# Kernel optimization log

Hardware: AMD Instinct MI355X
Metric: run time of the kernel (lower is better)

The kernel has to match this reference:

```python
import jax, jax.numpy as jnp
import numpy as np

E = 160000
N_NODES = 10000
AVG_NUM_NEIGHBORS = 16.0
INV_SQRT3 = 0.5773502691896258  # CG normalization for 1o x 1o -> 0e


def setup_inputs() -> dict:
    key = jax.random.key(0)
    ks = jax.random.split(key, 12)
    d = {
        "edge_s": jax.random.normal(ks[0], (E, 64), jnp.float32),
        "edge_v": jax.random.normal(ks[1], (E, 64, 3), jnp.float32),
        "attr_s": jax.random.normal(ks[2], (E, 1), jnp.float32),
        "attr_v": jax.random.normal(ks[3], (E, 3), jnp.float32),
        "W1": jax.random.normal(ks[4], (64, 128), jnp.float32) / np.sqrt(64),
        "b1": jnp.zeros((128,), jnp.float32),
        "W2": jax.random.normal(ks[5], (128, 128), jnp.float32) / np.sqrt(128),
        "b2": jnp.zeros((128,), jnp.float32),
        "Wg": jax.random.normal(ks[6], (128, 256), jnp.float32) / np.sqrt(128),
        "bg": jnp.zeros((256,), jnp.float32),
        "receivers": jax.random.randint(ks[7], (E,), 0, N_NODES, jnp.int32),
        "n_nodes": N_NODES,
    }
    return d


def reference(edge_s, edge_v, attr_s, attr_v, W1, b1, W2, b2, Wg, bg, receivers, n_nodes):
    # --- equivariant tensor product (filtered to 0e + 1o) ---
    # 0e outputs: [0e x 0e -> 0e (64)] ++ [1o x 1o -> 0e (64)]
    m0 = jnp.concatenate(
        [edge_s * attr_s,
         jnp.einsum("evc,ec->ev", edge_v, attr_v) * INV_SQRT3],
        axis=-1)                                            # [E, 128]
    # 1o outputs: [0e x 1o -> 1o (64)] ++ [1o x 0e -> 1o (64)]
    m1 = jnp.concatenate(
        [edge_s[:, :, None] * attr_v[:, None, :],
         edge_v * attr_s[:, :, None]],
        axis=1)                                             # [E, 128, 3]

    # --- scalar MLP gate (activate_final=True) + Linear to num_irreps=256 ---
    h = jax.nn.silu(edge_s @ W1 + b1)
    h = jax.nn.silu(h @ W2 + b2)
    gate = h @ Wg + bg                                      # [E, 256]
    g0, g1 = gate[:, :128], gate[:, 128:]

    m0 = m0 * g0
    m1 = m1 * g1[:, :, None]

    # --- scatter-add aggregation over receivers ---
    node0 = jax.ops.segment_sum(m0, receivers, num_segments=n_nodes)   # [N, 128]
    node1 = jax.ops.segment_sum(
        m1.reshape(m1.shape[0], -1), receivers, num_segments=n_nodes)  # [N, 384]

    out = jnp.concatenate([node0, node1], axis=-1)          # [N, 512]
    return out / jnp.sqrt(jnp.float32(AVG_NUM_NEIGHBORS))
```

## Files before the change

### kernel.cpp

```cpp
#include <hip/hip_runtime.h>
#include <math.h>

#define EPB 16
#define MEPB 32
#define NTHREADS 256
#define SCAN_T 1024
#define MAX_NODES_SCAN 10240
#define INV_SQRT3f 0.57735026918962584f
#define WFRAG_BYTES (112 * 1024)

typedef short bf16x8 __attribute__((ext_vector_type(8)));
typedef float f32x4  __attribute__((ext_vector_type(4)));

__device__ __forceinline__ float silu_f(float x) {
    return x * (1.0f / (1.0f + __expf(-x)));
}

__device__ __forceinline__ unsigned short f2bf(float f) {
    union { float f; unsigned u; } c; c.f = f;
    unsigned u = c.u + 0x7FFFu + ((c.u >> 16) & 1u);
    return (unsigned short)(u >> 16);
}

__global__ __launch_bounds__(64)
void wprep(const float* __restrict__ W1, const float* __restrict__ W2,
           const float* __restrict__ Wg, short* __restrict__ wf) {
    const int fid = blockIdx.x;
    const int l = threadIdx.x;
    const float* W; int N, nt, kt;
    if (fid < 16)      { W = W1; N = 128; nt = fid >> 1;        kt = fid & 1; }
    else if (fid < 48) { W = W2; N = 128; nt = (fid - 16) >> 2; kt = (fid - 16) & 3; }
    else               { W = Wg; N = 256; nt = (fid - 48) >> 2; kt = (fid - 48) & 3; }
    const int col = nt * 16 + (l & 15);
    const int k0  = kt * 32 + (l >> 4) * 8;
    short* out = wf + fid * 512 + l * 8;
    #pragma unroll
    for (int j = 0; j < 8; ++j)
        out[j] = (short)f2bf(W[(k0 + j) * N + col]);
}

__global__ __launch_bounds__(NTHREADS)
void mlp_gate_mfma(const float* __restrict__ edge_s,
                   const float* __restrict__ b1,
                   const float* __restrict__ b2,
                   const float* __restrict__ bg,
                   const short* __restrict__ wf,
                   float* __restrict__ gate_out,
                   int E)
{
    __shared__ alignas(16) char h_lds[2][32 * 256];

    const int tid = threadIdx.x;
    const int w  = tid >> 6;
    const int l  = tid & 63;
    const int lg = l >> 4;
    const int lc = l & 15;
    const long e0 = (long)blockIdx.x * MEPB;
    if (e0 + MEPB > E) return;

    bf16x8 a1[2][2];
    #pragma unroll
    for (int mt = 0; mt < 2; ++mt)
        #pragma unroll
        for (int kt = 0; kt < 2; ++kt) {
            const float* p = edge_s + (e0 + mt * 16 + lc) * 64 + kt * 32 + lg * 8;
            float4 x0 = *(const float4*)p;
            float4 x1 = *(const float4*)(p + 4);
            bf16x8 a;
            a[0] = (short)f2bf(x0.x); a[1] = (short)f2bf(x0.y);
            a[2] = (short)f2bf(x0.z); a[3] = (short)f2bf(x0.w);
            a[4] = (short)f2bf(x1.x); a[5] = (short)f2bf(x1.y);
            a[6] = (short)f2bf(x1.z); a[7] = (short)f2bf(x1.w);
            a1[mt][kt] = a;
        }

    {
        bf16x8 bw[2][2];
        #pragma unroll
        for (int nt = 0; nt < 2; ++nt)
            #pragma unroll
            for (int kt = 0; kt < 2; ++kt)
                bw[nt][kt] = *(const bf16x8*)(wf + ((2 * w + nt) * 2 + kt) * 512 + l * 8);

        f32x4 acc[2][2];
        #pragma unroll
        for (int mt = 0; mt < 2; ++mt)
            #pragma unroll
            for (int nt = 0; nt < 2; ++nt) {
                f32x4 c = {0.f, 0.f, 0.f, 0.f};
                #pragma unroll
                for (int kt = 0; kt < 2; ++kt)
                    c = __builtin_amdgcn_mfma_f32_16x16x32_bf16(a1[mt][kt], bw[nt][kt], c, 0, 0, 0);
                acc[mt][nt] = c;
            }

        #pragma unroll
        for (int nt = 0; nt < 2; ++nt) {
            float bb = b1[32 * w + nt * 16 + lc];
            int col2 = (32 * w + nt * 16 + lc) * 2;
            #pragma unroll
            for (int mt = 0; mt < 2; ++mt)
                #pragma unroll
                for (int r = 0; r < 4; ++r) {
                    int row = mt * 16 + lg * 4 + r;
                    int off = (row * 256 + col2) ^ ((row & 7) << 4);
                    *(unsigned short*)&h_lds[0][off] = f2bf(silu_f(acc[mt][nt][r] + bb));
                }
        }
    }
    __syncthreads();

    {
        bf16x8 a2[2][4];
        #pragma unroll
        for (int mt = 0; mt < 2; ++mt)
            #pragma unroll
            for (int kt = 0; kt < 4; ++kt) {
                int row = mt * 16 + lc;
                int off = (row * 256 + (kt * 32 + lg * 8) * 2) ^ ((row & 7) << 4);
                a2[mt][kt] = *(const bf16x8*)&h_lds[0][off];
            }

        f32x4 acc[2][2];
        #pragma unroll
        for (int mt = 0; mt < 2; ++mt)
            #pragma unroll
            for (int nt = 0; nt < 2; ++nt) { f32x4 z = {0.f,0.f,0.f,0.f}; acc[mt][nt] = z; }

        #pragma unroll
        for (int kt = 0; kt < 4; ++kt) {
            bf16x8 bw[2];
            #pragma unroll
            for (int nt = 0; nt < 2; ++nt)
                bw[nt] = *(const bf16x8*)(wf + (16 + (2 * w + nt) * 4 + kt) * 512 + l * 8);
            #pragma unroll
            for (int mt = 0; mt < 2; ++mt)
                #pragma unroll
                for (int nt = 0; nt < 2; ++nt)
                    acc[mt][nt] = __builtin_amdgcn_mfma_f32_16x16x32_bf16(a2[mt][kt], bw[nt], acc[mt][nt], 0, 0, 0);
        }

        #pragma unroll
        for (int nt = 0; nt < 2; ++nt) {
            float bb = b2[32 * w + nt * 16 + lc];
            int col2 = (32 * w + nt * 16 + lc) * 2;
            #pragma unroll
            for (int mt = 0; mt < 2; ++mt)
                #pragma unroll
                for (int r = 0; r < 4; ++r) {
                    int row = mt * 16 + lg * 4 + r;
                    int off = (row * 256 + col2) ^ ((row & 7) << 4);
                    *(unsigned short*)&h_lds[1][off] = f2bf(silu_f(acc[mt][nt][r] + bb));
                }
        }
    }
    __syncthreads();

    {
        bf16x8 a3[2][4];
        #pragma unroll
        for (int mt = 0; mt < 2; ++mt)
            #pragma unroll
            for (int kt = 0; kt < 4; ++kt) {
                int row = mt * 16 + lc;
                int off = (row * 256 + (kt * 32 + lg * 8) * 2) ^ ((row & 7) << 4);
                a3[mt][kt] = *(const bf16x8*)&h_lds[1][off];
            }

        f32x4 acc[2][4];
        #pragma unroll
        for (int mt = 0; mt < 2; ++mt)
            #pragma unroll
            for (int nt = 0; nt < 4; ++nt) { f32x4 z = {0.f,0.f,0.f,0.f}; acc[mt][nt] = z; }

        #pragma unroll
        for (int kt = 0; kt < 4; ++kt) {
            bf16x8 bw[4];
            #pragma unroll
            for (int nt = 0; nt < 4; ++nt)
                bw[nt] = *(const bf16x8*)(wf + (48 + (4 * w + nt) * 4 + kt) * 512 + l * 8);
            #pragma unroll
            for (int mt = 0; mt < 2; ++mt)
                #pragma unroll
                for (int nt = 0; nt < 4; ++nt)
                    acc[mt][nt] = __builtin_amdgcn_mfma_f32_16x16x32_bf16(a3[mt][kt], bw[nt], acc[mt][nt], 0, 0, 0);
        }

        #pragma unroll
        for (int nt = 0; nt < 4; ++nt) {
            int col = 64 * w + nt * 16 + lc;
            float bb = bg[col];
            #pragma unroll
            for (int mt = 0; mt < 2; ++mt)
                #pragma unroll
                for (int r = 0; r < 4; ++r) {
                    long e = e0 + mt * 16 + lg * 4 + r;
                    gate_out[e * 256 + col] = (acc[mt][nt][r] + bb) * 0.25f;
                }
        }
    }
}

__global__ void csr_hist(const int* __restrict__ recv, int* __restrict__ counts, int E) {
    int e = blockIdx.x * 256 + threadIdx.x;
    if (e < E) atomicAdd(&counts[recv[e]], 1);
}

__global__ __launch_bounds__(SCAN_T)
void csr_scan(const int* __restrict__ counts, int* __restrict__ offsets,
              int* __restrict__ cursor, int N) {
    __shared__ int s_cnt[MAX_NODES_SCAN];
    __shared__ int s_ps[SCAN_T];
    const int t = threadIdx.x;
    for (int i = t; i < N; i += SCAN_T) s_cnt[i] = counts[i];
    __syncthreads();
    const int CH = (N + SCAN_T - 1) / SCAN_T;
    const int base = t * CH;
    int tsum = 0;
    for (int k = 0; k < CH; ++k) { int i = base + k; if (i < N) tsum += s_cnt[i]; }
    s_ps[t] = tsum;
    __syncthreads();
    for (int off = 1; off < SCAN_T; off <<= 1) {
        int v = (t >= off) ? s_ps[t - off] : 0;
        __syncthreads();
        s_ps[t] += v;
        __syncthreads();
    }
    int run = (t == 0) ? 0 : s_ps[t - 1];
    for (int k = 0; k < CH; ++k) {
        int i = base + k;
        if (i < N) { int c = s_cnt[i]; offsets[i] = run; cursor[i] = run; run += c; }
    }
    if (t == 0) offsets[N] = s_ps[SCAN_T - 1];
}

__global__ void csr_scatter(const int* __restrict__ recv, int* __restrict__ cursor,
                            int* __restrict__ eids, int E) {
    int e = blockIdx.x * 256 + threadIdx.x;
    if (e < E) {
        int p = atomicAdd(&cursor[recv[e]], 1);
        eids[p] = e;
    }
}

__global__ __launch_bounds__(NTHREADS)
void node_gather(const float* __restrict__ edge_s,
                 const float* __restrict__ edge_v,
                 const float* __restrict__ attr_s,
                 const float* __restrict__ attr_v,
                 const float* __restrict__ gate,
                 const int*   __restrict__ offsets,
                 const int*   __restrict__ eids,
                 float* __restrict__ out)
{
    __shared__ int s_ids[NTHREADS];
    const int n   = blockIdx.x;
    const int tid = threadIdx.x;
    const int start = offsets[n];
    const int end   = offsets[n + 1];
    const int i = tid - 128;

    float  acc0 = 0.0f;
    float3 acc1 = make_float3(0.0f, 0.0f, 0.0f);

    for (int base = start; base < end; base += NTHREADS) {
        const int cnt = min(NTHREADS, end - base);
        __syncthreads();
        if (tid < cnt) s_ids[tid] = eids[base + tid];
        __syncthreads();
        for (int p = 0; p < cnt; ++p) {
            const int e = s_ids[p];
            const float as  = attr_s[e];
            const float av0 = attr_v[e * 3 + 0];
            const float av1 = attr_v[e * 3 + 1];
            const float av2 = attr_v[e * 3 + 2];
            const float g   = gate[(size_t)e * 256 + tid];
            if (tid < 64) {
                acc0 = fmaf(edge_s[(size_t)e * 64 + tid] * as, g, acc0);
            } else if (tid < 128) {
                const float* ev = &edge_v[((size_t)e * 64 + (tid - 64)) * 3];
                float val = (ev[0] * av0 + ev[1] * av1 + ev[2] * av2) * INV_SQRT3f;
                acc0 = fmaf(val, g, acc0);
            } else if (i < 64) {
                float es = edge_s[(size_t)e * 64 + i];
                acc1.x = fmaf(es * av0, g, acc1.x);
                acc1.y = fmaf(es * av1, g, acc1.y);
                acc1.z = fmaf(es * av2, g, acc1.z);
            } else {
                const float* ev = &edge_v[((size_t)e * 64 + (i - 64)) * 3];
                acc1.x = fmaf(ev[0] * as, g, acc1.x);
                acc1.y = fmaf(ev[1] * as, g, acc1.y);
                acc1.z = fmaf(ev[2] * as, g, acc1.z);
            }
        }
    }

    float* orow = out + (size_t)n * 512;
    if (tid < 128) {
        orow[tid] = acc0;
    } else {
        orow[128 + 3 * i + 0] = acc1.x;
        orow[128 + 3 * i + 1] = acc1.y;
        orow[128 + 3 * i + 2] = acc1.z;
    }
}

__global__ __launch_bounds__(NTHREADS)
void mpconv_fused_atomic(const float* __restrict__ edge_s,
                         const float* __restrict__ edge_v,
                         const float* __restrict__ attr_s,
                         const float* __restrict__ attr_v,
                         const float* __restrict__ W1, const float* __restrict__ b1,
                         const float* __restrict__ W2, const float* __restrict__ b2,
                         const float* __restrict__ Wg, const float* __restrict__ bg,
                         const int*   __restrict__ recv,
                         float* __restrict__ out)
{
    __shared__ float s_esT[64][20];
    __shared__ float s_h1T[128][20];
    __shared__ float s_h2T[128][20];
    __shared__ float s_as[EPB];
    __shared__ float s_av[EPB][3];
    __shared__ int   s_r[EPB];

    const int tid = threadIdx.x;
    const long e0 = (long)blockIdx.x * EPB;

    for (int idx = tid; idx < EPB * 64; idx += NTHREADS) {
        int e = idx >> 6, k = idx & 63;
        s_esT[k][e] = edge_s[(e0 + e) * 64 + k];
    }
    if (tid < EPB) { s_as[tid] = attr_s[e0 + tid]; s_r[tid] = recv[e0 + tid]; }
    if (tid >= 64 && tid < 64 + EPB * 3) {
        int q = tid - 64; int e = q / 3, c = q - e * 3;
        s_av[e][c] = attr_v[(e0 + e) * 3 + c];
    }
    __syncthreads();

    const int j  = tid & 127;
    const int eg = (tid >> 7) << 3;
    {
        float acc[8];
        #pragma unroll
        for (int e = 0; e < 8; ++e) acc[e] = 0.0f;
        #pragma unroll 4
        for (int k = 0; k < 64; ++k) {
            float w  = W1[k * 128 + j];
            float4 a = *(const float4*)&s_esT[k][eg];
            float4 b = *(const float4*)&s_esT[k][eg + 4];
            acc[0] = fmaf(a.x, w, acc[0]); acc[1] = fmaf(a.y, w, acc[1]);
            acc[2] = fmaf(a.z, w, acc[2]); acc[3] = fmaf(a.w, w, acc[3]);
            acc[4] = fmaf(b.x, w, acc[4]); acc[5] = fmaf(b.y, w, acc[5]);
            acc[6] = fmaf(b.z, w, acc[6]); acc[7] = fmaf(b.w, w, acc[7]);
        }
        float bb = b1[j];
        float4 r0, r1;
        r0.x = silu_f(acc[0] + bb); r0.y = silu_f(acc[1] + bb);
        r0.z = silu_f(acc[2] + bb); r0.w = silu_f(acc[3] + bb);
        r1.x = silu_f(acc[4] + bb); r1.y = silu_f(acc[5] + bb);
        r1.z = silu_f(acc[6] + bb); r1.w = silu_f(acc[7] + bb);
        *(float4*)&s_h1T[j][eg]     = r0;
        *(float4*)&s_h1T[j][eg + 4] = r1;
    }
    __syncthreads();
    {
        float acc[8];
        #pragma unroll
        for (int e = 0; e < 8; ++e) acc[e] = 0.0f;
        #pragma unroll 4
        for (int k = 0; k < 128; ++k) {
            float w  = W2[k * 128 + j];
            float4 a = *(const float4*)&s_h1T[k][eg];
            float4 b = *(const float4*)&s_h1T[k][eg + 4];
            acc[0] = fmaf(a.x, w, acc[0]); acc[1] = fmaf(a.y, w, acc[1]);
            acc[2] = fmaf(a.z, w, acc[2]); acc[3] = fmaf(a.w, w, acc[3]);
            acc[4] = fmaf(b.x, w, acc[4]); acc[5] = fmaf(b.y, w, acc[5]);
            acc[6] = fmaf(b.z, w, acc[6]); acc[7] = fmaf(b.w, w, acc[7]);
        }
        float bb = b2[j];
        float4 r0, r1;
        r0.x = silu_f(acc[0] + bb); r0.y = silu_f(acc[1] + bb);
        r0.z = silu_f(acc[2] + bb); r0.w = silu_f(acc[3] + bb);
        r1.x = silu_f(acc[4] + bb); r1.y = silu_f(acc[5] + bb);
        r1.z = silu_f(acc[6] + bb); r1.w = silu_f(acc[7] + bb);
        *(float4*)&s_h2T[j][eg]     = r0;
        *(float4*)&s_h2T[j][eg + 4] = r1;
    }
    __syncthreads();
    float g[EPB];
    {
        float acc[16];
        #pragma unroll
        for (int e = 0; e < 16; ++e) acc[e] = 0.0f;
        #pragma unroll 2
        for (int k = 0; k < 128; ++k) {
            float w = Wg[k * 256 + tid];
            float4 a0 = *(const float4*)&s_h2T[k][0];
            float4 a1 = *(const float4*)&s_h2T[k][4];
            float4 a2 = *(const float4*)&s_h2T[k][8];
            float4 a3 = *(const float4*)&s_h2T[k][12];
            acc[0]  = fmaf(a0.x, w, acc[0]);  acc[1]  = fmaf(a0.y, w, acc[1]);
            acc[2]  = fmaf(a0.z, w, acc[2]);  acc[3]  = fmaf(a0.w, w, acc[3]);
            acc[4]  = fmaf(a1.x, w, acc[4]);  acc[5]  = fmaf(a1.y, w, acc[5]);
            acc[6]  = fmaf(a1.z, w, acc[6]);  acc[7]  = fmaf(a1.w, w, acc[7]);
            acc[8]  = fmaf(a2.x, w, acc[8]);  acc[9]  = fmaf(a2.y, w, acc[9]);
            acc[10] = fmaf(a2.z, w, acc[10]); acc[11] = fmaf(a2.w, w, acc[11]);
            acc[12] = fmaf(a3.x, w, acc[12]); acc[13] = fmaf(a3.y, w, acc[13]);
            acc[14] = fmaf(a3.z, w, acc[14]); acc[15] = fmaf(a3.w, w, acc[15]);
        }
        float bb = bg[tid];
        #pragma unroll
        for (int e = 0; e < 16; ++e) g[e] = (acc[e] + bb) * 0.25f;
    }
    if (tid < 128) {
        const int jj = tid;
        #pragma unroll 4
        for (int e = 0; e < EPB; ++e) {
            float val;
            if (jj < 64) {
                val = s_esT[jj][e] * s_as[e];
            } else {
                const float* ev = &edge_v[((e0 + e) * 64 + (jj - 64)) * 3];
                val = (ev[0] * s_av[e][0] + ev[1] * s_av[e][1] + ev[2] * s_av[e][2]) * INV_SQRT3f;
            }
            atomicAdd(&out[(long)s_r[e] * 512 + jj], val * g[e]);
        }
    } else {
        const int ii = tid - 128;
        #pragma unroll 4
        for (int e = 0; e < EPB; ++e) {
            float mx, my, mz;
            if (ii < 64) {
                float es = s_esT[ii][e];
                mx = es * s_av[e][0]; my = es * s_av[e][1]; mz = es * s_av[e][2];
            } else {
                const float* ev = &edge_v[((e0 + e) * 64 + (ii - 64)) * 3];
                float as = s_as[e];
                mx = ev[0] * as; my = ev[1] * as; mz = ev[2] * as;
            }
            float* o = &out[(long)s_r[e] * 512 + 128 + ii * 3];
            atomicAdd(o + 0, mx * g[e]);
            atomicAdd(o + 1, my * g[e]);
            atomicAdd(o + 2, mz * g[e]);
        }
    }
}

extern "C" void kernel_launch(void* const* d_in, const int* in_sizes, int n_in,
                              void* d_out, int out_size, void* d_ws, size_t ws_size,
                              hipStream_t stream) {
    const float* edge_s = (const float*)d_in[0];
    const float* edge_v = (const float*)d_in[1];
    const float* attr_s = (const float*)d_in[2];
    const float* attr_v = (const float*)d_in[3];
    const float* W1     = (const float*)d_in[4];
    const float* b1     = (const float*)d_in[5];
    const float* W2     = (const float*)d_in[6];
    const float* b2     = (const float*)d_in[7];
    const float* Wg     = (const float*)d_in[8];
    const float* bg     = (const float*)d_in[9];
    const int*   recv   = (const int*)d_in[10];

    const int E = in_sizes[0] / 64;
    const int N = out_size / 512;

    const size_t gate_bytes = (size_t)E * 256 * sizeof(float);
    const size_t int_count  = (size_t)N + (size_t)(N + 1) + (size_t)N + (size_t)E;
    const size_t needed = gate_bytes + WFRAG_BYTES + int_count * sizeof(int);

    if (ws_size < needed || N > MAX_NODES_SCAN || (E % MEPB) != 0) {
        hipMemsetAsync(d_out, 0, (size_t)out_size * sizeof(float), stream);
        mpconv_fused_atomic<<<(E + EPB - 1) / EPB, NTHREADS, 0, stream>>>(
            edge_s, edge_v, attr_s, attr_v, W1, b1, W2, b2, Wg, bg, recv,
            (float*)d_out);
        return;
    }

    float* gate    = (float*)d_ws;
    short* wfrags  = (short*)((char*)d_ws + gate_bytes);
    int*   counts  = (int*)((char*)d_ws + gate_bytes + WFRAG_BYTES);
    int*   offsets = counts + N;
    int*   cursor  = offsets + (N + 1);
    int*   eids    = cursor + N;

    hipMemsetAsync(counts, 0, (size_t)N * sizeof(int), stream);
    wprep      <<<112, 64, 0, stream>>>(W1, W2, Wg, wfrags);
    csr_hist   <<<(E + 255) / 256, 256, 0, stream>>>(recv, counts, E);
    csr_scan   <<<1, SCAN_T, 0, stream>>>(counts, offsets, cursor, N);
    csr_scatter<<<(E + 255) / 256, 256, 0, stream>>>(recv, cursor, eids, E);
    mlp_gate_mfma<<<E / MEPB, NTHREADS, 0, stream>>>(edge_s, b1, b2, bg,
                                                     wfrags, gate, E);
    node_gather<<<N, NTHREADS, 0, stream>>>(edge_s, edge_v, attr_s, attr_v,
                                            gate, offsets, eids, (float*)d_out);
}
```

Before: 380.3 us.

## Store gate intermediate in bf16 and batch edge loads in node gather

The gate tensor written by the MLP kernel and read by the gather kernel is stored as bf16 instead of fp32, which halves that intermediate's write and read traffic. The node gather loop is restructured per wavefront to load eight edges' operands at a time before accumulating, giving more memory-level parallelism and removing per-thread divergent branches. Rounding the gate to bf16 adds precision loss in the output.

After: 374.9 us. No clear change (-1.4%).

```diff
diff --git a/kernel.cpp b/kernel.cpp
--- a/kernel.cpp
+++ b/kernel.cpp
@@ -20,6 +20,10 @@
     union { float f; unsigned u; } c; c.f = f;
     unsigned u = c.u + 0x7FFFu + ((c.u >> 16) & 1u);
     return (unsigned short)(u >> 16);
+}
+
+__device__ __forceinline__ float bf2f(unsigned short h) {
+    union { unsigned u; float f; } c; c.u = ((unsigned)h) << 16; return c.f;
 }
 
 __global__ __launch_bounds__(64)
@@ -45,7 +49,7 @@
                    const float* __restrict__ b2,
                    const float* __restrict__ bg,
                    const short* __restrict__ wf,
-                   float* __restrict__ gate_out,
+                   unsigned short* __restrict__ gate_out,
                    int E)
 {
     __shared__ alignas(16) char h_lds[2][32 * 256];
@@ -195,7 +199,7 @@
                 #pragma unroll
                 for (int r = 0; r < 4; ++r) {
                     long e = e0 + mt * 16 + lg * 4 + r;
-                    gate_out[e * 256 + col] = (acc[mt][nt][r] + bb) * 0.25f;
+                    gate_out[e * 256 + col] = f2bf((acc[mt][nt][r] + bb) * 0.25f);
                 }
         }
     }
@@ -248,17 +252,18 @@
                  const float* __restrict__ edge_v,
                  const float* __restrict__ attr_s,
                  const float* __restrict__ attr_v,
-                 const float* __restrict__ gate,
+                 const unsigned short* __restrict__ gate,
                  const int*   __restrict__ offsets,
                  const int*   __restrict__ eids,
                  float* __restrict__ out)
 {
     __shared__ int s_ids[NTHREADS];
-    const int n   = blockIdx.x;
-    const int tid = threadIdx.x;
+    const int n    = blockIdx.x;
+    const int tid  = threadIdx.x;
+    const int w    = tid >> 6;
+    const int lane = tid & 63;
     const int start = offsets[n];
     const int end   = offsets[n + 1];
-    const int i = tid - 128;
 
     float  acc0 = 0.0f;
     float3 acc1 = make_float3(0.0f, 0.0f, 0.0f);
@@ -268,29 +273,73 @@
         __syncthreads();
         if (tid < cnt) s_ids[tid] = eids[base + tid];
         __syncthreads();
-        for (int p = 0; p < cnt; ++p) {
-            const int e = s_ids[p];
-            const float as  = attr_s[e];
-            const float av0 = attr_v[e * 3 + 0];
-            const float av1 = attr_v[e * 3 + 1];
-            const float av2 = attr_v[e * 3 + 2];
-            const float g   = gate[(size_t)e * 256 + tid];
-            if (tid < 64) {
-                acc0 = fmaf(edge_s[(size_t)e * 64 + tid] * as, g, acc0);
-            } else if (tid < 128) {
-                const float* ev = &edge_v[((size_t)e * 64 + (tid - 64)) * 3];
-                float val = (ev[0] * av0 + ev[1] * av1 + ev[2] * av2) * INV_SQRT3f;
-                acc0 = fmaf(val, g, acc0);
-            } else if (i < 64) {
-                float es = edge_s[(size_t)e * 64 + i];
-                acc1.x = fmaf(es * av0, g, acc1.x);
-                acc1.y = fmaf(es * av1, g, acc1.y);
-                acc1.z = fmaf(es * av2, g, acc1.z);
+
+        for (int p = 0; p < cnt; p += 8) {
+            const int m = min(8, cnt - p);
+            float gv[8];
+            if (w == 0) {
+                float mv[8];
+                #pragma unroll
+                for (int q = 0; q < 8; ++q) {
+                    if (q < m) {
+                        const int e = s_ids[p + q];
+                        gv[q] = bf2f(gate[(size_t)e * 256 + tid]);
+                        mv[q] = edge_s[(size_t)e * 64 + lane] * attr_s[e];
+                    } else { gv[q] = 0.0f; mv[q] = 0.0f; }
+                }
+                #pragma unroll
+                for (int q = 0; q < 8; ++q) acc0 = fmaf(mv[q], gv[q], acc0);
+            } else if (w == 1) {
+                float mv[8];
+                #pragma unroll
+                for (int q = 0; q < 8; ++q) {
+                    if (q < m) {
+                        const int e = s_ids[p + q];
+                        gv[q] = bf2f(gate[(size_t)e * 256 + tid]);
+                        const float* ev = &edge_v[((size_t)e * 64 + lane) * 3];
+                        mv[q] = (ev[0] * attr_v[e * 3 + 0] + ev[1] * attr_v[e * 3 + 1]
+                               + ev[2] * attr_v[e * 3 + 2]) * INV_SQRT3f;
+                    } else { gv[q] = 0.0f; mv[q] = 0.0f; }
+                }
+                #pragma unroll
+                for (int q = 0; q < 8; ++q) acc0 = fmaf(mv[q], gv[q], acc0);
+            } else if (w == 2) {
+                float mx[8], my[8], mz[8];
+                #pragma unroll
+                for (int q = 0; q < 8; ++q) {
+                    if (q < m) {
+                        const int e = s_ids[p + q];
+                        gv[q] = bf2f(gate[(size_t)e * 256 + tid]);
+                        const float es = edge_s[(size_t)e * 64 + lane];
+                        mx[q] = es * attr_v[e * 3 + 0];
+                        my[q] = es * attr_v[e * 3 + 1];
+                        mz[q] = es * attr_v[e * 3 + 2];
+                    } else { gv[q] = 0.0f; mx[q] = my[q] = mz[q] = 0.0f; }
+                }
+                #pragma unroll
+                for (int q = 0; q < 8; ++q) {
+                    acc1.x = fmaf(mx[q], gv[q], acc1.x);
+                    acc1.y = fmaf(my[q], gv[q], acc1.y);
+                    acc1.z = fmaf(mz[q], gv[q], acc1.z);
+                }
             } else {
-                const float* ev = &edge_v[((size_t)e * 64 + (i - 64)) * 3];
-                acc1.x = fmaf(ev[0] * as, g, acc1.x);
-                acc1.y = fmaf(ev[1] * as, g, acc1.y);
-                acc1.z = fmaf(ev[2] * as, g, acc1.z);
+                float mx[8], my[8], mz[8];
+                #pragma unroll
+                for (int q = 0; q < 8; ++q) {
+                    if (q < m) {
+                        const int e = s_ids[p + q];
+                        gv[q] = bf2f(gate[(size_t)e * 256 + tid]);
+                        const float* ev = &edge_v[((size_t)e * 64 + lane) * 3];
+                        const float as = attr_s[e];
+                        mx[q] = ev[0] * as; my[q] = ev[1] * as; mz[q] = ev[2] * as;
+                    } else { gv[q] = 0.0f; mx[q] = my[q] = mz[q] = 0.0f; }
+                }
+                #pragma unroll
+                for (int q = 0; q < 8; ++q) {
+                    acc1.x = fmaf(mx[q], gv[q], acc1.x);
+                    acc1.y = fmaf(my[q], gv[q], acc1.y);
+                    acc1.z = fmaf(mz[q], gv[q], acc1.z);
+                }
             }
         }
     }
@@ -299,6 +348,7 @@
     if (tid < 128) {
         orow[tid] = acc0;
     } else {
+        const int i = tid - 128;
         orow[128 + 3 * i + 0] = acc1.x;
         orow[128 + 3 * i + 1] = acc1.y;
         orow[128 + 3 * i + 2] = acc1.z;
@@ -464,7 +514,7 @@
     const int E = in_sizes[0] / 64;
     const int N = out_size / 512;
 
-    const size_t gate_bytes = (size_t)E * 256 * sizeof(float);
+    const size_t gate_bytes = (size_t)E * 256 * sizeof(unsigned short);
     const size_t int_count  = (size_t)N + (size_t)(N + 1) + (size_t)N + (size_t)E;
     const size_t needed = gate_bytes + WFRAG_BYTES + int_count * sizeof(int);
 
@@ -476,7 +526,7 @@
         return;
     }
 
-    float* gate    = (float*)d_ws;
+    unsigned short* gate = (unsigned short*)d_ws;
     short* wfrags  = (short*)((char*)d_ws + gate_bytes);
     int*   counts  = (int*)((char*)d_ws + gate_bytes + WFRAG_BYTES);
     int*   offsets = counts + N;
```

## Store gate as bf16 in CSR order and stage edge rows in LDS

Applied to the files above, without the earlier changes.

The MLP kernel now writes gate values as bf16 into rows permuted by each edge's CSR rank, so node_gather reads the gate contiguously instead of through an indirect index. node_gather also stages groups of 8 edges' edge_s, edge_v and attr data in shared memory using coalesced float4 loads, replacing per-thread strided gathers. This halves gate traffic and improves access patterns at the cost of bf16 rounding on the gate and scattered stores in the MLP kernel.

Result: no change. 384.7 us (+1.2%).

```diff
diff --git a/kernel.cpp b/kernel.cpp
--- a/kernel.cpp
+++ b/kernel.cpp
@@ -6,6 +6,7 @@
 #define NTHREADS 256
 #define SCAN_T 1024
 #define MAX_NODES_SCAN 10240
+#define GC 8
 #define INV_SQRT3f 0.57735026918962584f
 #define WFRAG_BYTES (112 * 1024)
 
@@ -20,6 +21,10 @@
     union { float f; unsigned u; } c; c.f = f;
     unsigned u = c.u + 0x7FFFu + ((c.u >> 16) & 1u);
     return (unsigned short)(u >> 16);
+}
+
+__device__ __forceinline__ float bf2f(unsigned short h) {
+    union { unsigned u; float f; } c; c.u = ((unsigned)h) << 16; return c.f;
 }
 
 __global__ __launch_bounds__(64)
@@ -45,7 +50,8 @@
                    const float* __restrict__ b2,
                    const float* __restrict__ bg,
                    const short* __restrict__ wf,
-                   float* __restrict__ gate_out,
+                   const int*   __restrict__ rank,
+                   unsigned short* __restrict__ gate_out,
                    int E)
 {
     __shared__ alignas(16) char h_lds[2][32 * 256];
@@ -74,6 +80,13 @@
             a1[mt][kt] = a;
         }
 
+    int rowIdx[2][4];
+    #pragma unroll
+    for (int mt = 0; mt < 2; ++mt)
+        #pragma unroll
+        for (int r = 0; r < 4; ++r)
+            rowIdx[mt][r] = rank[e0 + mt * 16 + lg * 4 + r];
+
     {
         bf16x8 bw[2][2];
         #pragma unroll
@@ -193,10 +206,9 @@
             #pragma unroll
             for (int mt = 0; mt < 2; ++mt)
                 #pragma unroll
-                for (int r = 0; r < 4; ++r) {
-                    long e = e0 + mt * 16 + lg * 4 + r;
-                    gate_out[e * 256 + col] = (acc[mt][nt][r] + bb) * 0.25f;
-                }
+                for (int r = 0; r < 4; ++r)
+                    gate_out[(size_t)rowIdx[mt][r] * 256 + col] =
+                        f2bf((acc[mt][nt][r] + bb) * 0.25f);
         }
     }
 }
@@ -235,11 +247,12 @@
 }
 
 __global__ void csr_scatter(const int* __restrict__ recv, int* __restrict__ cursor,
-                            int* __restrict__ eids, int E) {
+                            int* __restrict__ eids, int* __restrict__ rank, int E) {
     int e = blockIdx.x * 256 + threadIdx.x;
     if (e < E) {
         int p = atomicAdd(&cursor[recv[e]], 1);
         eids[p] = e;
+        rank[e] = p;
     }
 }
 
@@ -248,17 +261,23 @@
                  const float* __restrict__ edge_v,
                  const float* __restrict__ attr_s,
                  const float* __restrict__ attr_v,
-                 const float* __restrict__ gate,
+                 const unsigned short* __restrict__ gate,
                  const int*   __restrict__ offsets,
                  const int*   __restrict__ eids,
                  float* __restrict__ out)
 {
-    __shared__ int s_ids[NTHREADS];
-    const int n   = blockIdx.x;
-    const int tid = threadIdx.x;
+    __shared__ int   s_ids[NTHREADS];
+    __shared__ float s_es[GC][64];
+    __shared__ float s_ev[GC][192];
+    __shared__ float s_as[GC];
+    __shared__ float s_av[GC][3];
+
+    const int n    = blockIdx.x;
+    const int tid  = threadIdx.x;
+    const int w    = tid >> 6;
+    const int lane = tid & 63;
     const int start = offsets[n];
     const int end   = offsets[n + 1];
-    const int i = tid - 128;
 
     float  acc0 = 0.0f;
     float3 acc1 = make_float3(0.0f, 0.0f, 0.0f);
@@ -268,30 +287,59 @@
         __syncthreads();
         if (tid < cnt) s_ids[tid] = eids[base + tid];
         __syncthreads();
-        for (int p = 0; p < cnt; ++p) {
-            const int e = s_ids[p];
-            const float as  = attr_s[e];
-            const float av0 = attr_v[e * 3 + 0];
-            const float av1 = attr_v[e * 3 + 1];
-            const float av2 = attr_v[e * 3 + 2];
-            const float g   = gate[(size_t)e * 256 + tid];
-            if (tid < 64) {
-                acc0 = fmaf(edge_s[(size_t)e * 64 + tid] * as, g, acc0);
-            } else if (tid < 128) {
-                const float* ev = &edge_v[((size_t)e * 64 + (tid - 64)) * 3];
-                float val = (ev[0] * av0 + ev[1] * av1 + ev[2] * av2) * INV_SQRT3f;
-                acc0 = fmaf(val, g, acc0);
-            } else if (i < 64) {
-                float es = edge_s[(size_t)e * 64 + i];
-                acc1.x = fmaf(es * av0, g, acc1.x);
-                acc1.y = fmaf(es * av1, g, acc1.y);
-                acc1.z = fmaf(es * av2, g, acc1.z);
-            } else {
-                const float* ev = &edge_v[((size_t)e * 64 + (i - 64)) * 3];
-                acc1.x = fmaf(ev[0] * as, g, acc1.x);
-                acc1.y = fmaf(ev[1] * as, g, acc1.y);
-                acc1.z = fmaf(ev[2] * as, g, acc1.z);
-            }
+
+        for (int p = 0; p < cnt; p += GC) {
+            const int m = min(GC, cnt - p);
+
+            for (int u = tid; u < 512; u += NTHREADS) {
+                if (u < 128) {
+                    int q = u >> 4;
+                    if (q < m) {
+                        int e = s_ids[p + q];
+                        ((float4*)s_es[q])[u & 15] =
+                            ((const float4*)(edge_s + (size_t)e * 64))[u & 15];
+                    }
+                } else {
+                    int u2 = u - 128;
+                    int q = u2 / 48, part = u2 - q * 48;
+                    if (q < m) {
+                        int e = s_ids[p + q];
+                        ((float4*)s_ev[q])[part] =
+                            ((const float4*)(edge_v + (size_t)e * 192))[part];
+                    }
+                }
+            }
+            if (tid < m) s_as[tid] = attr_s[s_ids[p + tid]];
+            if (tid >= 64 && tid < 64 + 3 * m) {
+                int q = (tid - 64) / 3, c = (tid - 64) - q * 3;
+                s_av[q][c] = attr_v[s_ids[p + q] * 3 + c];
+            }
+            __syncthreads();
+
+            #pragma unroll 4
+            for (int q = 0; q < m; ++q) {
+                const float g = bf2f(gate[(size_t)(base + p + q) * 256 + tid]);
+                if (w == 0) {
+                    acc0 = fmaf(s_es[q][lane] * s_as[q], g, acc0);
+                } else if (w == 1) {
+                    const float* ev = &s_ev[q][lane * 3];
+                    float mv = (ev[0] * s_av[q][0] + ev[1] * s_av[q][1]
+                              + ev[2] * s_av[q][2]) * INV_SQRT3f;
+                    acc0 = fmaf(mv, g, acc0);
+                } else if (w == 2) {
+                    const float es = s_es[q][lane];
+                    acc1.x = fmaf(es * s_av[q][0], g, acc1.x);
+                    acc1.y = fmaf(es * s_av[q][1], g, acc1.y);
+                    acc1.z = fmaf(es * s_av[q][2], g, acc1.z);
+                } else {
+                    const float* ev = &s_ev[q][lane * 3];
+                    const float as = s_as[q];
+                    acc1.x = fmaf(ev[0] * as, g, acc1.x);
+                    acc1.y = fmaf(ev[1] * as, g, acc1.y);
+                    acc1.z = fmaf(ev[2] * as, g, acc1.z);
+                }
+            }
+            __syncthreads();
         }
     }
 
@@ -299,6 +347,7 @@
     if (tid < 128) {
         orow[tid] = acc0;
     } else {
+        const int i = tid - 128;
         orow[128 + 3 * i + 0] = acc1.x;
         orow[128 + 3 * i + 1] = acc1.y;
         orow[128 + 3 * i + 2] = acc1.z;
@@ -464,8 +513,9 @@
     const int E = in_sizes[0] / 64;
     const int N = out_size / 512;
 
-    const size_t gate_bytes = (size_t)E * 256 * sizeof(float);
-    const size_t int_count  = (size_t)N + (size_t)(N + 1) + (size_t)N + (size_t)E;
+    const size_t gate_bytes = (size_t)E * 256 * sizeof(unsigned short);
+    const size_t int_count  = (size_t)N + (size_t)(N + 1) + (size_t)N
+                            + (size_t)E  + (size_t)E ;
     const size_t needed = gate_bytes + WFRAG_BYTES + int_count * sizeof(int);
 
     if (ws_size < needed || N > MAX_NODES_SCAN || (E % MEPB) != 0) {
@@ -476,20 +526,21 @@
         return;
     }
 
-    float* gate    = (float*)d_ws;
+    unsigned short* gate = (unsigned short*)d_ws;
     short* wfrags  = (short*)((char*)d_ws + gate_bytes);
     int*   counts  = (int*)((char*)d_ws + gate_bytes + WFRAG_BYTES);
     int*   offsets = counts + N;
     int*   cursor  = offsets + (N + 1);
     int*   eids    = cursor + N;
+    int*   rank    = eids + E;
 
     hipMemsetAsync(counts, 0, (size_t)N * sizeof(int), stream);
     wprep      <<<112, 64, 0, stream>>>(W1, W2, Wg, wfrags);
     csr_hist   <<<(E + 255) / 256, 256, 0, stream>>>(recv, counts, E);
     csr_scan   <<<1, SCAN_T, 0, stream>>>(counts, offsets, cursor, N);
-    csr_scatter<<<(E + 255) / 256, 256, 0, stream>>>(recv, cursor, eids, E);
+    csr_scatter<<<(E + 255) / 256, 256, 0, stream>>>(recv, cursor, eids, rank, E);
     mlp_gate_mfma<<<E / MEPB, NTHREADS, 0, stream>>>(edge_s, b1, b2, bg,
-                                                     wfrags, gate, E);
+                                                     wfrags, rank, gate, E);
     node_gather<<<N, NTHREADS, 0, stream>>>(edge_s, edge_v, attr_s, attr_v,
                                             gate, offsets, eids, (float*)d_out);
 }
```
